# Kernel optimization log

Hardware: AMD Instinct MI355X
Metric: run time of the kernel (lower is better)

Reference implementation:

```python
import jax, jax.numpy as jnp
import numpy as np

B, S, D, H = 16, 2048, 512, 64


def setup_inputs() -> dict:
    key = jax.random.key(0)
    k_in, kq, kk, kv = jax.random.split(key, 4)
    scale = 1.0 / np.sqrt(D)
    return {
        "inputs": jax.random.normal(k_in, (B, S, D), dtype=jnp.float32),
        "Wq": jax.random.normal(kq, (D, H), dtype=jnp.float32) * scale,
        "bq": jnp.zeros((H,), dtype=jnp.float32),
        "Wk": jax.random.normal(kk, (D, H), dtype=jnp.float32) * scale,
        "bk": jnp.zeros((H,), dtype=jnp.float32),
        "Wv": jax.random.normal(kv, (D, H), dtype=jnp.float32) * scale,
        "bv": jnp.zeros((H,), dtype=jnp.float32),
    }


def reference(inputs, Wq, bq, Wk, bk, Wv, bv):
    # Q, K, V projections: [B,S,D] @ [D,H] -> [B,S,H]
    q = inputs @ Wq + bq
    k = inputs @ Wk + bk
    v = inputs @ Wv + bv
    # scaled dot-product attention scores: [B,S,S]
    scores = jnp.einsum("bsh,bth->bst", q, k) / jnp.sqrt(jnp.float32(H))
    weights = jax.nn.softmax(scores, axis=-1)
    # context: [B,S,H]
    context = jnp.einsum("bst,bth->bsh", weights, v)
    # mean pool over sequence -> [B,H]
    return jnp.mean(context, axis=1)
```

## Files before the change

### kernel.cpp

```cpp
#include <hip/hip_runtime.h>
#include <hip/hip_bf16.h>

#define B_ 16
#define S_ 2048
#define D_ 512
#define H_ 64

typedef __attribute__((ext_vector_type(8))) short short8;
typedef __attribute__((ext_vector_type(4))) float f32x4;
typedef __attribute__((ext_vector_type(16))) float f32x16;

static __device__ __forceinline__ short f2bf(float f) {
  union { __hip_bfloat16 h; short s; } u;
  u.h = __float2bfloat16(f);
  return u.s;
}

static __device__ __forceinline__ unsigned cvtpk(float lo, float hi) {
  unsigned r;
  asm("v_cvt_pk_bf16_f32 %0, %1, %2" : "=v"(r) : "v"(lo), "v"(hi));
  return r;
}

__global__ void prep_weights(const float* __restrict__ Wq,
                             const float* __restrict__ Wk,
                             const float* __restrict__ Wv,
                             const float* __restrict__ bq,
                             const float* __restrict__ bk,
                             const float* __restrict__ bv,
                             short* __restrict__ Wt, float* __restrict__ biasAll) {
  int n = blockIdx.x;
  const float* src  = (n < 64) ? Wq : (n < 128) ? Wk : Wv;
  const float* bsrc = (n < 64) ? bq : (n < 128) ? bk : bv;
  int col = n & 63;
  for (int k = threadIdx.x; k < D_; k += 256)
    Wt[n * D_ + k] = f2bf(src[k * H_ + col]);
  if (threadIdx.x == 0) biasAll[n] = bsrc[col];
}

__global__ __launch_bounds__(384) void qkv_proj(
    const float* __restrict__ in, const short* __restrict__ Wt,
    const float* __restrict__ biasAll,
    short* __restrict__ Qb, short* __restrict__ Kb, short* __restrict__ Vt) {
  int tid = threadIdx.x;
  int w = tid >> 6, l = tid & 63, cl = l & 31, h = l >> 5;
  int rh = w & 1, ct = w >> 1;
  int rowbase = blockIdx.x * 64;

  const float* ap = in + (size_t)(rowbase + rh * 32 + cl) * D_;
  const short* wb0 = Wt + (ct * 64 + cl) * D_ + h * 8;
  const short* wb1 = wb0 + 32 * D_;
  float bias0 = biasAll[ct * 64 + cl];
  float bias1 = biasAll[ct * 64 + 32 + cl];

  f32x16 a0, a1;
#pragma unroll
  for (int i = 0; i < 16; ++i) { a0[i] = 0.f; a1[i] = 0.f; }

#pragma unroll 4
  for (int ks = 0; ks < 32; ++ks) {
    int off = ks * 16 + h * 8;
    float4 f0 = *reinterpret_cast<const float4*>(ap + off);
    float4 f1 = *reinterpret_cast<const float4*>(ap + off + 4);
    union { unsigned u[4]; short8 v; } af;
    af.u[0] = cvtpk(f0.x, f0.y);
    af.u[1] = cvtpk(f0.z, f0.w);
    af.u[2] = cvtpk(f1.x, f1.y);
    af.u[3] = cvtpk(f1.z, f1.w);
    short8 b0 = *reinterpret_cast<const short8*>(wb0 + ks * 16);
    short8 b1 = *reinterpret_cast<const short8*>(wb1 + ks * 16);
    a0 = __builtin_amdgcn_mfma_f32_32x32x16_bf16(af.v, b0, a0, 0, 0, 0);
    a1 = __builtin_amdgcn_mfma_f32_32x32x16_bf16(af.v, b1, a1, 0, 0, 0);
  }

  int b = rowbase >> 11, srow0 = rowbase & (S_ - 1);
#pragma unroll
  for (int i = 0; i < 16; ++i) {
    int rl = (i & 3) + 8 * (i >> 2) + 4 * h + rh * 32;
    size_t grow = (size_t)(rowbase + rl);
    short v0 = f2bf(a0[i] + bias0);
    short v1 = f2bf(a1[i] + bias1);
    if (ct == 0) {
      Qb[grow * H_ + cl] = v0;
      Qb[grow * H_ + 32 + cl] = v1;
    } else if (ct == 1) {
      Kb[grow * H_ + cl] = v0;
      Kb[grow * H_ + 32 + cl] = v1;
    } else {
      Vt[((size_t)b * H_ + cl) * S_ + srow0 + rl] = v0;
      Vt[((size_t)b * H_ + 32 + cl) * S_ + srow0 + rl] = v1;
    }
  }
}

__global__ __launch_bounds__(256, 4) void attn_pool(
    const short* __restrict__ Qb, const short* __restrict__ Kb,
    const short* __restrict__ Vt, float* __restrict__ out) {
  int tid = threadIdx.x;
  int w = tid >> 6, l = tid & 63, q = l & 31, h = l >> 5;
  int qc = blockIdx.x & 63, b = blockIdx.x >> 6;
  size_t boff = (size_t)b * (S_ * H_);
  int qrow = qc * 32;

  const float c = 0.18033688011112042f;

  short8 qa[4];
#pragma unroll
  for (int s4 = 0; s4 < 4; ++s4)
    qa[s4] = *reinterpret_cast<const short8*>(
        Qb + boff + (size_t)(qrow + q) * H_ + s4 * 16 + h * 8);

  f32x16 o0, o1;
#pragma unroll
  for (int i = 0; i < 16; ++i) { o0[i] = 0.f; o1[i] = 0.f; }
  float m = -INFINITY, lsum = 0.f;

  const short* vbase = Vt + ((size_t)b * H_ + q) * S_;

  for (int it = 0; it < 16; ++it) {
    int tbase = w * 512 + it * 32;

    const short* kp = Kb + boff + (size_t)(tbase + q) * H_ + h * 8;
    f32x16 st;
#pragma unroll
    for (int i = 0; i < 16; ++i) st[i] = 0.f;
#pragma unroll
    for (int s4 = 0; s4 < 4; ++s4) {
      short8 ka = *reinterpret_cast<const short8*>(kp + s4 * 16);
      st = __builtin_amdgcn_mfma_f32_32x32x16_bf16(ka, qa[s4], st, 0, 0, 0);
    }

    float tm = st[0];
#pragma unroll
    for (int i = 1; i < 16; ++i) tm = fmaxf(tm, st[i]);
    tm = fmaxf(tm, __shfl_xor(tm, 32));
    float mn = fmaxf(m, tm);
    float cmn = mn * c;
    float al = exp2f(m * c - cmn);
    float p[16];
    float ts = 0.f;
#pragma unroll
    for (int i = 0; i < 16; ++i) {
      p[i] = exp2f(st[i] * c - cmn);
      ts += p[i];
    }
    ts += __shfl_xor(ts, 32);
    lsum = lsum * al + ts;
    m = mn;
#pragma unroll
    for (int i = 0; i < 16; ++i) { o0[i] *= al; o1[i] *= al; }

    unsigned W[4][2];
#pragma unroll
    for (int t = 0; t < 4; ++t) {
      W[t][0] = cvtpk(p[4 * t + 0], p[4 * t + 1]);
      W[t][1] = cvtpk(p[4 * t + 2], p[4 * t + 3]);
    }
    short8 bf[2];
#pragma unroll
    for (int s = 0; s < 2; ++s) {
      unsigned k0 = h ? W[2 * s + 1][0] : W[2 * s][0];
      unsigned k1 = h ? W[2 * s + 1][1] : W[2 * s][1];
      unsigned s0 = h ? W[2 * s][0] : W[2 * s + 1][0];
      unsigned s1 = h ? W[2 * s][1] : W[2 * s + 1][1];
      unsigned r0 = (unsigned)__shfl_xor((int)s0, 32);
      unsigned r1 = (unsigned)__shfl_xor((int)s1, 32);
      union { unsigned u[4]; short8 v; } bb;
      bb.u[0] = h ? r0 : k0;
      bb.u[1] = h ? r1 : k1;
      bb.u[2] = h ? k0 : r0;
      bb.u[3] = h ? k1 : r1;
      bf[s] = bb.v;
    }

    const short* vp = vbase + tbase + h * 8;
#pragma unroll
    for (int s = 0; s < 2; ++s) {
      short8 va0 = *reinterpret_cast<const short8*>(vp + s * 16);
      short8 va1 = *reinterpret_cast<const short8*>(vp + 32 * S_ + s * 16);
      o0 = __builtin_amdgcn_mfma_f32_32x32x16_bf16(va0, bf[s], o0, 0, 0, 0);
      o1 = __builtin_amdgcn_mfma_f32_32x32x16_bf16(va1, bf[s], o1, 0, 0, 0);
    }
  }

  float sc = exp2f(m * c);

  __shared__ float mo[4][64][33];
  __shared__ float mls[4][32];
  __shared__ float red[4][64];
#pragma unroll
  for (int i = 0; i < 16; ++i) {
    int dv = (i & 3) + 8 * (i >> 2) + 4 * h;
    mo[w][dv][q] = o0[i] * sc;
    mo[w][32 + dv][q] = o1[i] * sc;
  }
  if (h == 0) mls[w][q] = lsum * sc;
  __syncthreads();

  int dv = tid & 63, qg = tid >> 6;
  float acc = 0.f;
#pragma unroll
  for (int j = 0; j < 8; ++j) {
    int qq = qg * 8 + j;
    float L = mls[0][qq] + mls[1][qq] + mls[2][qq] + mls[3][qq];
    float num = mo[0][dv][qq] + mo[1][dv][qq] + mo[2][dv][qq] + mo[3][dv][qq];
    acc += num / L;
  }
  red[qg][dv] = acc;
  __syncthreads();
  if (tid < 64) {
    float s = red[0][tid] + red[1][tid] + red[2][tid] + red[3][tid];
    atomicAdd(out + b * H_ + tid, s * (1.0f / (float)S_));
  }
}

extern "C" void kernel_launch(void* const* d_in, const int* in_sizes, int n_in,
                              void* d_out, int out_size, void* d_ws, size_t ws_size,
                              hipStream_t stream) {
  const float* in = (const float*)d_in[0];
  const float* Wq = (const float*)d_in[1];
  const float* bq = (const float*)d_in[2];
  const float* Wk = (const float*)d_in[3];
  const float* bk = (const float*)d_in[4];
  const float* Wv = (const float*)d_in[5];
  const float* bv = (const float*)d_in[6];
  float* out = (float*)d_out;

  char* ws = (char*)d_ws;
  short* Qb      = (short*)(ws);
  short* Kb      = (short*)(ws + (size_t)4 * 1024 * 1024);
  short* Vt      = (short*)(ws + (size_t)8 * 1024 * 1024);
  short* Wt      = (short*)(ws + (size_t)12 * 1024 * 1024);
  float* biasAll = (float*)(ws + (size_t)12 * 1024 * 1024 + 192 * 1024);

  prep_weights<<<192, 256, 0, stream>>>(Wq, Wk, Wv, bq, bk, bv, Wt, biasAll);
  qkv_proj<<<512, 384, 0, stream>>>(in, Wt, biasAll, Qb, Kb, Vt);
  hipMemsetAsync(d_out, 0, (size_t)out_size * sizeof(float), stream);
  attn_pool<<<1024, 256, 0, stream>>>(Qb, Kb, Vt, out);
}
```

Baseline: 210.6 us.

## Restructure QKV projection with LDS staging and prefetch K/V in attention

The QKV projection now stages each 32-row input tile in swizzled LDS as bf16, shared by six waves that each compute one 32-column slice, and writes V transposed through an LDS tile with vectorized stores. The softmax scale (including log2e) is folded into Wq and bq, which removes per-element multiplies. The attention loop is fully unrolled, prefetches the next K tile and the V tile ahead of the MFMAs, wraps the MFMAs in s_setprio, and rescales the running max only when it grows by more than 8. The partial-output LDS buffer is stored as bf16. Together these add precision loss, from bf16 partials and exp values up to 2^8 before rescaling, plus register pressure from the unroll and prefetch, since the occupancy hint was dropped.

```diff
diff --git a/kernel.cpp b/kernel.cpp
--- a/kernel.cpp
+++ b/kernel.cpp
@@ -7,7 +7,6 @@
 #define H_ 64
 
 typedef __attribute__((ext_vector_type(8))) short short8;
-typedef __attribute__((ext_vector_type(4))) float f32x4;
 typedef __attribute__((ext_vector_type(16))) float f32x16;
 
 static __device__ __forceinline__ short f2bf(float f) {
@@ -15,7 +14,11 @@
   u.h = __float2bfloat16(f);
   return u.s;
 }
-
+static __device__ __forceinline__ float b2f(short s) {
+  union { float f; unsigned u; } x;
+  x.u = ((unsigned)(unsigned short)s) << 16;
+  return x.f;
+}
 static __device__ __forceinline__ unsigned cvtpk(float lo, float hi) {
   unsigned r;
   asm("v_cvt_pk_bf16_f32 %0, %1, %2" : "=v"(r) : "v"(lo), "v"(hi));
@@ -32,10 +35,11 @@
   int n = blockIdx.x;
   const float* src  = (n < 64) ? Wq : (n < 128) ? Wk : Wv;
   const float* bsrc = (n < 64) ? bq : (n < 128) ? bk : bv;
+  float scale = (n < 64) ? 0.18033688011112042f : 1.0f;
   int col = n & 63;
   for (int k = threadIdx.x; k < D_; k += 256)
-    Wt[n * D_ + k] = f2bf(src[k * H_ + col]);
-  if (threadIdx.x == 0) biasAll[n] = bsrc[col];
+    Wt[n * D_ + k] = f2bf(src[k * H_ + col] * scale);
+  if (threadIdx.x == 0) biasAll[n] = bsrc[col] * scale;
 }
 
 __global__ __launch_bounds__(384) void qkv_proj(
@@ -44,56 +48,67 @@
     short* __restrict__ Qb, short* __restrict__ Kb, short* __restrict__ Vt) {
   int tid = threadIdx.x;
   int w = tid >> 6, l = tid & 63, cl = l & 31, h = l >> 5;
-  int rh = w & 1, ct = w >> 1;
-  int rowbase = blockIdx.x * 64;
-
-  const float* ap = in + (size_t)(rowbase + rh * 32 + cl) * D_;
-  const short* wb0 = Wt + (ct * 64 + cl) * D_ + h * 8;
-  const short* wb1 = wb0 + 32 * D_;
-  float bias0 = biasAll[ct * 64 + cl];
-  float bias1 = biasAll[ct * 64 + 32 + cl];
-
-  f32x16 a0, a1;
-#pragma unroll
-  for (int i = 0; i < 16; ++i) { a0[i] = 0.f; a1[i] = 0.f; }
-
-#pragma unroll 4
+  int rowbase = blockIdx.x * 32;
+
+  __shared__ short alds[16384];
+  __shared__ short vtile[64][40];
+
+  if (tid < 256) {
+#pragma unroll
+    for (int itr = 0; itr < 8; ++itr) {
+      int i = itr * 256 + tid;
+      int r = i >> 6, c8 = i & 63;
+      const float* sp = in + (size_t)(rowbase + r) * D_ + c8 * 8;
+      float4 f0 = *reinterpret_cast<const float4*>(sp);
+      float4 f1 = *reinterpret_cast<const float4*>(sp + 4);
+      union { unsigned u[4]; short8 v; } pk;
+      pk.u[0] = cvtpk(f0.x, f0.y); pk.u[1] = cvtpk(f0.z, f0.w);
+      pk.u[2] = cvtpk(f1.x, f1.y); pk.u[3] = cvtpk(f1.z, f1.w);
+      int addr = r * 1024 + ((c8 * 16) ^ ((r & 7) << 4));
+      *reinterpret_cast<short8*>(reinterpret_cast<char*>(alds) + addr) = pk.v;
+    }
+  }
+  __syncthreads();
+
+  const short* wb = Wt + (w * 32 + cl) * D_ + h * 8;
+  f32x16 acc;
+#pragma unroll
+  for (int i = 0; i < 16; ++i) acc[i] = 0.f;
+  int abase = cl * 1024, axor = (cl & 7) << 4;
+#pragma unroll 8
   for (int ks = 0; ks < 32; ++ks) {
-    int off = ks * 16 + h * 8;
-    float4 f0 = *reinterpret_cast<const float4*>(ap + off);
-    float4 f1 = *reinterpret_cast<const float4*>(ap + off + 4);
-    union { unsigned u[4]; short8 v; } af;
-    af.u[0] = cvtpk(f0.x, f0.y);
-    af.u[1] = cvtpk(f0.z, f0.w);
-    af.u[2] = cvtpk(f1.x, f1.y);
-    af.u[3] = cvtpk(f1.z, f1.w);
-    short8 b0 = *reinterpret_cast<const short8*>(wb0 + ks * 16);
-    short8 b1 = *reinterpret_cast<const short8*>(wb1 + ks * 16);
-    a0 = __builtin_amdgcn_mfma_f32_32x32x16_bf16(af.v, b0, a0, 0, 0, 0);
-    a1 = __builtin_amdgcn_mfma_f32_32x32x16_bf16(af.v, b1, a1, 0, 0, 0);
-  }
-
-  int b = rowbase >> 11, srow0 = rowbase & (S_ - 1);
-#pragma unroll
-  for (int i = 0; i < 16; ++i) {
-    int rl = (i & 3) + 8 * (i >> 2) + 4 * h + rh * 32;
-    size_t grow = (size_t)(rowbase + rl);
-    short v0 = f2bf(a0[i] + bias0);
-    short v1 = f2bf(a1[i] + bias1);
-    if (ct == 0) {
-      Qb[grow * H_ + cl] = v0;
-      Qb[grow * H_ + 32 + cl] = v1;
-    } else if (ct == 1) {
-      Kb[grow * H_ + cl] = v0;
-      Kb[grow * H_ + 32 + cl] = v1;
-    } else {
-      Vt[((size_t)b * H_ + cl) * S_ + srow0 + rl] = v0;
-      Vt[((size_t)b * H_ + 32 + cl) * S_ + srow0 + rl] = v1;
-    }
-  }
-}
-
-__global__ __launch_bounds__(256, 4) void attn_pool(
+    short8 af = *reinterpret_cast<const short8*>(
+        reinterpret_cast<char*>(alds) + abase + ((ks * 32 + h * 16) ^ axor));
+    short8 bf = *reinterpret_cast<const short8*>(wb + ks * 16);
+    acc = __builtin_amdgcn_mfma_f32_32x32x16_bf16(af, bf, acc, 0, 0, 0);
+  }
+
+  float bias = biasAll[w * 32 + cl];
+  if (w < 4) {
+    short* dst = (w < 2) ? Qb : Kb;
+    int cb = (w & 1) * 32 + cl;
+#pragma unroll
+    for (int i = 0; i < 16; ++i) {
+      int rl = (i & 3) + 8 * (i >> 2) + 4 * h;
+      dst[(size_t)(rowbase + rl) * H_ + cb] = f2bf(acc[i] + bias);
+    }
+  } else {
+#pragma unroll
+    for (int i = 0; i < 16; ++i) {
+      int rl = (i & 3) + 8 * (i >> 2) + 4 * h;
+      vtile[(w - 4) * 32 + cl][rl] = f2bf(acc[i] + bias);
+    }
+  }
+  __syncthreads();
+  if (tid < 256) {
+    int hh = tid >> 2, ch = tid & 3;
+    short8 v = *reinterpret_cast<const short8*>(&vtile[hh][ch * 8]);
+    int b = rowbase >> 11, s0 = rowbase & (S_ - 1);
+    *reinterpret_cast<short8*>(Vt + ((size_t)b * H_ + hh) * S_ + s0 + ch * 8) = v;
+  }
+}
+
+__global__ __launch_bounds__(256) void attn_pool(
     const short* __restrict__ Qb, const short* __restrict__ Kb,
     const short* __restrict__ Vt, float* __restrict__ out) {
   int tid = threadIdx.x;
@@ -102,8 +117,6 @@
   size_t boff = (size_t)b * (S_ * H_);
   int qrow = qc * 32;
 
-  const float c = 0.18033688011112042f;
-
   short8 qa[4];
 #pragma unroll
   for (int s4 = 0; s4 < 4; ++s4)
@@ -115,47 +128,69 @@
   for (int i = 0; i < 16; ++i) { o0[i] = 0.f; o1[i] = 0.f; }
   float m = -INFINITY, lsum = 0.f;
 
-  const short* vbase = Vt + ((size_t)b * H_ + q) * S_;
-
+  const short* vrow = Vt + ((size_t)b * H_ + q) * S_;
+
+  short8 ka[4];
+  {
+    const short* kp = Kb + boff + (size_t)(w * 512 + q) * H_ + h * 8;
+#pragma unroll
+    for (int s4 = 0; s4 < 4; ++s4)
+      ka[s4] = *reinterpret_cast<const short8*>(kp + s4 * 16);
+  }
+
+#pragma unroll
   for (int it = 0; it < 16; ++it) {
     int tbase = w * 512 + it * 32;
 
-    const short* kp = Kb + boff + (size_t)(tbase + q) * H_ + h * 8;
+    const short* vp = vrow + tbase + h * 8;
+    short8 va0 = *reinterpret_cast<const short8*>(vp);
+    short8 va1 = *reinterpret_cast<const short8*>(vp + 16);
+    short8 va2 = *reinterpret_cast<const short8*>(vp + 32 * S_);
+    short8 va3 = *reinterpret_cast<const short8*>(vp + 32 * S_ + 16);
+    short8 kn[4];
+    if (it < 15) {
+      const short* kp = Kb + boff + (size_t)(tbase + 32 + q) * H_ + h * 8;
+#pragma unroll
+      for (int s4 = 0; s4 < 4; ++s4)
+        kn[s4] = *reinterpret_cast<const short8*>(kp + s4 * 16);
+    }
+
     f32x16 st;
 #pragma unroll
     for (int i = 0; i < 16; ++i) st[i] = 0.f;
-#pragma unroll
-    for (int s4 = 0; s4 < 4; ++s4) {
-      short8 ka = *reinterpret_cast<const short8*>(kp + s4 * 16);
-      st = __builtin_amdgcn_mfma_f32_32x32x16_bf16(ka, qa[s4], st, 0, 0, 0);
-    }
+    __builtin_amdgcn_s_setprio(1);
+#pragma unroll
+    for (int s4 = 0; s4 < 4; ++s4)
+      st = __builtin_amdgcn_mfma_f32_32x32x16_bf16(ka[s4], qa[s4], st, 0, 0, 0);
+    __builtin_amdgcn_s_setprio(0);
 
     float tm = st[0];
 #pragma unroll
     for (int i = 1; i < 16; ++i) tm = fmaxf(tm, st[i]);
     tm = fmaxf(tm, __shfl_xor(tm, 32));
-    float mn = fmaxf(m, tm);
-    float cmn = mn * c;
-    float al = exp2f(m * c - cmn);
-    float p[16];
+    if (__any(tm > m + 8.0f)) {
+      float mn = fmaxf(m, tm);
+      float al = exp2f(m - mn);
+      lsum *= al;
+#pragma unroll
+      for (int i = 0; i < 16; ++i) { o0[i] *= al; o1[i] *= al; }
+      m = mn;
+    }
     float ts = 0.f;
-#pragma unroll
-    for (int i = 0; i < 16; ++i) {
-      p[i] = exp2f(st[i] * c - cmn);
-      ts += p[i];
+    unsigned W[4][2];
+#pragma unroll
+    for (int t = 0; t < 4; ++t) {
+      float p0 = exp2f(st[4 * t + 0] - m);
+      float p1 = exp2f(st[4 * t + 1] - m);
+      float p2 = exp2f(st[4 * t + 2] - m);
+      float p3 = exp2f(st[4 * t + 3] - m);
+      ts += (p0 + p1) + (p2 + p3);
+      W[t][0] = cvtpk(p0, p1);
+      W[t][1] = cvtpk(p2, p3);
     }
     ts += __shfl_xor(ts, 32);
-    lsum = lsum * al + ts;
-    m = mn;
-#pragma unroll
-    for (int i = 0; i < 16; ++i) { o0[i] *= al; o1[i] *= al; }
-
-    unsigned W[4][2];
-#pragma unroll
-    for (int t = 0; t < 4; ++t) {
-      W[t][0] = cvtpk(p[4 * t + 0], p[4 * t + 1]);
-      W[t][1] = cvtpk(p[4 * t + 2], p[4 * t + 3]);
-    }
+    lsum += ts;
+
     short8 bf[2];
 #pragma unroll
     for (int s = 0; s < 2; ++s) {
@@ -173,26 +208,29 @@
       bf[s] = bb.v;
     }
 
-    const short* vp = vbase + tbase + h * 8;
-#pragma unroll
-    for (int s = 0; s < 2; ++s) {
-      short8 va0 = *reinterpret_cast<const short8*>(vp + s * 16);
-      short8 va1 = *reinterpret_cast<const short8*>(vp + 32 * S_ + s * 16);
-      o0 = __builtin_amdgcn_mfma_f32_32x32x16_bf16(va0, bf[s], o0, 0, 0, 0);
-      o1 = __builtin_amdgcn_mfma_f32_32x32x16_bf16(va1, bf[s], o1, 0, 0, 0);
-    }
-  }
-
-  float sc = exp2f(m * c);
-
-  __shared__ float mo[4][64][33];
+    __builtin_amdgcn_s_setprio(1);
+    o0 = __builtin_amdgcn_mfma_f32_32x32x16_bf16(va0, bf[0], o0, 0, 0, 0);
+    o0 = __builtin_amdgcn_mfma_f32_32x32x16_bf16(va1, bf[1], o0, 0, 0, 0);
+    o1 = __builtin_amdgcn_mfma_f32_32x32x16_bf16(va2, bf[0], o1, 0, 0, 0);
+    o1 = __builtin_amdgcn_mfma_f32_32x32x16_bf16(va3, bf[1], o1, 0, 0, 0);
+    __builtin_amdgcn_s_setprio(0);
+
+    if (it < 15) {
+#pragma unroll
+      for (int s4 = 0; s4 < 4; ++s4) ka[s4] = kn[s4];
+    }
+  }
+
+  float sc = exp2f(m);
+
+  __shared__ short mo[4][64][34];
   __shared__ float mls[4][32];
   __shared__ float red[4][64];
 #pragma unroll
   for (int i = 0; i < 16; ++i) {
     int dv = (i & 3) + 8 * (i >> 2) + 4 * h;
-    mo[w][dv][q] = o0[i] * sc;
-    mo[w][32 + dv][q] = o1[i] * sc;
+    mo[w][dv][q] = f2bf(o0[i] * sc);
+    mo[w][32 + dv][q] = f2bf(o1[i] * sc);
   }
   if (h == 0) mls[w][q] = lsum * sc;
   __syncthreads();
@@ -203,7 +241,8 @@
   for (int j = 0; j < 8; ++j) {
     int qq = qg * 8 + j;
     float L = mls[0][qq] + mls[1][qq] + mls[2][qq] + mls[3][qq];
-    float num = mo[0][dv][qq] + mo[1][dv][qq] + mo[2][dv][qq] + mo[3][dv][qq];
+    float num = b2f(mo[0][dv][qq]) + b2f(mo[1][dv][qq]) +
+                b2f(mo[2][dv][qq]) + b2f(mo[3][dv][qq]);
     acc += num / L;
   }
   red[qg][dv] = acc;
@@ -234,7 +273,7 @@
   float* biasAll = (float*)(ws + (size_t)12 * 1024 * 1024 + 192 * 1024);
 
   prep_weights<<<192, 256, 0, stream>>>(Wq, Wk, Wv, bq, bk, bv, Wt, biasAll);
-  qkv_proj<<<512, 384, 0, stream>>>(in, Wt, biasAll, Qb, Kb, Vt);
+  qkv_proj<<<1024, 384, 0, stream>>>(in, Wt, biasAll, Qb, Kb, Vt);
   hipMemsetAsync(d_out, 0, (size_t)out_size * sizeof(float), stream);
   attn_pool<<<1024, 256, 0, stream>>>(Qb, Kb, Vt, out);
 }
```

Result: faster. 189.5 us (-10.0%).
